# Kernel optimization log

Hardware: AMD Instinct MI355X
Metric: run time of the kernel (lower is better)

## Reference

```python
import jax, jax.numpy as jnp
import numpy as np

B, S, D_IN, D_OUT, H = 4, 2048, 1024, 1024, 16
HD = D_OUT // H  # 64


def setup_inputs() -> dict:
    key = jax.random.key(0)
    ks = jax.random.split(key, 6)
    s = 1.0 / np.sqrt(D_IN)
    return {
        "x": jax.random.normal(ks[0], (B, S, D_IN), dtype=jnp.float32),
        "Wq": jax.random.uniform(ks[1], (D_IN, D_OUT), jnp.float32, -s, s),
        "Wk": jax.random.uniform(ks[2], (D_IN, D_OUT), jnp.float32, -s, s),
        "Wv": jax.random.uniform(ks[3], (D_IN, D_OUT), jnp.float32, -s, s),
        "Wo": jax.random.uniform(ks[4], (D_OUT, D_OUT), jnp.float32, -s, s),
        "bo": jax.random.uniform(ks[5], (D_OUT,), jnp.float32, -s, s),
    }


def reference(x, Wq, Wk, Wv, Wo, bo):
    b, s, _ = x.shape
    # QKV projections -> [b, H, s, hd]
    def split_heads(t):
        return t.reshape(b, s, H, HD).transpose(0, 2, 1, 3)
    q = split_heads(x @ Wq)
    k = split_heads(x @ Wk)
    v = split_heads(x @ Wv)
    # attention scores [b, H, s, s]
    scores = jnp.einsum("bhqd,bhkd->bhqk", q, k)
    causal = jnp.triu(jnp.ones((s, s), dtype=bool), k=1)
    scores = jnp.where(causal, -jnp.inf, scores)
    attn = jax.nn.softmax(scores / np.sqrt(HD), axis=-1)
    ctx = jnp.einsum("bhqk,bhkd->bhqd", attn, v)
    ctx = ctx.transpose(0, 2, 1, 3).reshape(b, s, D_OUT)
    return ctx @ Wo + bo
```

## Files before the change

### kernel.cpp

```cpp
#include <hip/hip_runtime.h>

typedef __attribute__((ext_vector_type(8))) short bf16x8;
typedef __attribute__((ext_vector_type(4))) float f32x4;
typedef __attribute__((ext_vector_type(4))) unsigned uint4v;

#define SM_C 0.18033688011112042f
#define SM_M 20.0f
#define MFMA16 __builtin_amdgcn_mfma_f32_16x16x32_bf16

__device__ __forceinline__ unsigned short f2bf(float f) {
  unsigned u = __builtin_bit_cast(unsigned, f);
  u += 0x7fffu + ((u >> 16) & 1u);
  return (unsigned short)(u >> 16);
}

__device__ __forceinline__ unsigned cvtpk(float lo, float hi) {
  unsigned r;
  asm volatile("v_cvt_pk_bf16_f32 %0, %1, %2" : "=v"(r) : "v"(lo), "v"(hi));
  return r;
}

__device__ __forceinline__ void gload16(const void* g, void* lds) {
  __builtin_amdgcn_global_load_lds(
      (const __attribute__((address_space(1))) void*)g,
      (__attribute__((address_space(3))) void*)lds, 16, 0, 0);
}

#define BARRIER __builtin_amdgcn_s_barrier()
#define LGKM0 asm volatile("s_waitcnt lgkmcnt(0)" ::: "memory")
#define VM0 asm volatile("s_waitcnt vmcnt(0)" ::: "memory")

__global__ __launch_bounds__(256) void prep(const float* __restrict__ x,
                                            unsigned short* __restrict__ xb,
                                            const float* __restrict__ W0,
                                            const float* __restrict__ W1,
                                            const float* __restrict__ W2,
                                            const float* __restrict__ W3,
                                            unsigned short* __restrict__ WT) {
  __shared__ float tile[32][33];
  const int bid = blockIdx.x;
  if (bid < 2048) {
    int i = bid * 256 + threadIdx.x;
    for (; i < 2097152; i += 2048 * 256) {
      float4 v = ((const float4*)x)[i];
      unsigned long long packed = (unsigned long long)f2bf(v.x) |
                                  ((unsigned long long)f2bf(v.y) << 16) |
                                  ((unsigned long long)f2bf(v.z) << 32) |
                                  ((unsigned long long)f2bf(v.w) << 48);
      ((unsigned long long*)xb)[i] = packed;
    }
  } else {
    int b2 = bid - 2048;
    const int z = b2 >> 10;
    b2 &= 1023;
    const int bx = b2 & 31, by = b2 >> 5;
    const float* W = (z == 0) ? W0 : (z == 1) ? W1 : (z == 2) ? W2 : W3;
    unsigned short* WTo = WT + (size_t)z * 1048576;
    const int tx = threadIdx.x & 31, ty = threadIdx.x >> 5;
    const int xcol = bx * 32 + tx;
    for (int i = 0; i < 4; ++i) {
      int r = ty + i * 8;
      tile[r][tx] = W[(by * 32 + r) * 1024 + xcol];
    }
    __syncthreads();
    const int nx = by * 32 + tx;
    for (int i = 0; i < 4; ++i) {
      int r = ty + i * 8;
      WTo[(long)(bx * 32 + r) * 1024 + nx] = f2bf(tile[tx][r]);
    }
  }
}

template <int MODE>
__global__ __launch_bounds__(256) void gemm97(const unsigned short* __restrict__ A,
                                              const unsigned short* __restrict__ BT,
                                              unsigned short* __restrict__ Cb,
                                              float* __restrict__ Cf,
                                              const float* __restrict__ bias,
                                              int M, int N, int K) {
  __shared__ alignas(16) unsigned short As[2][128 * 64];
  __shared__ alignas(16) unsigned short Bs[2][128 * 64];

  const int nbn = N >> 7;
  const int tmg = (M >> 7) >> 3;
  const int cc = blockIdx.x >> 3, xc = blockIdx.x & 7;
  const int tm = xc * tmg + cc / nbn, tn = cc % nbn;

  const int t = threadIdx.x, l = t & 63, wid = t >> 6;
  const int wm = wid >> 1, wn = wid & 1;
  const int lr = l & 15, lg = l >> 4;

  f32x4 acc[4][4] = {};

  const int sq = t >> 3;
  const int sslot8 = ((t & 7) ^ (sq & 7)) * 8;
  const unsigned short* Ath = A + ((long)tm * 128 + sq) * K + sslot8;
  const unsigned short* Bth = BT + ((long)tn * 128 + sq) * K + sslot8;
  const int ldsoff = sq * 64 + (t & 7) * 8;

#define STG(buf, kt)                                                      \
  do {                                                                    \
    _Pragma("unroll") for (int q_ = 0; q_ < 4; ++q_) {                    \
      gload16(Ath + (long)(q_ * 32) * K + (kt) * 64,                      \
              &As[buf][q_ * 2048 + ldsoff]);                              \
      gload16(Bth + (long)(q_ * 32) * K + (kt) * 64,                      \
              &Bs[buf][q_ * 2048 + ldsoff]);                              \
    }                                                                     \
  } while (0)

  const int NT = K >> 6;
  STG(0, 0);
  VM0;
  BARRIER;

  const int offk0 = (lg ^ (lr & 7)) * 8;
  const int offk1 = ((4 + lg) ^ (lr & 7)) * 8;
  const int arow0 = (wm * 64 + lr) * 64;
  const int brow0 = (wn * 64 + lr) * 64;

  for (int tt = 0; tt < NT; ++tt) {
    const int cur = tt & 1;
    if (tt + 1 < NT) STG(cur ^ 1, tt + 1);

    const unsigned short* Ac = As[cur];
    const unsigned short* Bc = Bs[cur];
    bf16x8 af[4][2], bfr[4][2];
#pragma unroll
    for (int m = 0; m < 4; ++m) {
      const unsigned short* ap = Ac + arow0 + m * 1024;
      af[m][0] = *(const bf16x8*)(ap + offk0);
      af[m][1] = *(const bf16x8*)(ap + offk1);
    }
#pragma unroll
    for (int n = 0; n < 4; ++n) {
      const unsigned short* bp = Bc + brow0 + n * 1024;
      bfr[n][0] = *(const bf16x8*)(bp + offk0);
      bfr[n][1] = *(const bf16x8*)(bp + offk1);
    }
    LGKM0;
    __builtin_amdgcn_s_setprio(1);
#pragma unroll
    for (int m = 0; m < 4; ++m)
#pragma unroll
      for (int n = 0; n < 4; ++n) {
        acc[m][n] = MFMA16(af[m][0], bfr[n][0], acc[m][n], 0, 0, 0);
        acc[m][n] = MFMA16(af[m][1], bfr[n][1], acc[m][n], 0, 0, 0);
      }
    __builtin_amdgcn_s_setprio(0);

    if (tt + 1 < NT) {
      VM0;
      BARRIER;
    }
  }
#undef STG

  const long crow = (long)tm * 128 + wm * 64;
  const int ccolw = wn * 64;

  if constexpr (MODE == 1) {
#pragma unroll
    for (int m = 0; m < 4; ++m)
#pragma unroll
      for (int n = 0; n < 4; ++n)
#pragma unroll
        for (int r = 0; r < 4; ++r) {
          long row = crow + m * 16 + lg * 4 + r;
          int col = tn * 128 + ccolw + n * 16 + lr;
          Cf[row * N + col] = acc[m][n][r] + bias[col];
        }
  } else {
    if (tn < 16) {
      unsigned short* pl = Cb + ((tn < 8) ? 0 : 8388608);
      const int pc = (tn & 7) * 128 + ccolw + lr;
#pragma unroll
      for (int m = 0; m < 4; ++m)
#pragma unroll
        for (int n = 0; n < 4; ++n)
#pragma unroll
          for (int r = 0; r < 4; ++r) {
            long row = crow + m * 16 + lg * 4 + r;
            pl[row * 1024 + pc + n * 16] = f2bf(acc[m][n][r]);
          }
    } else {
      unsigned short* VtW = Cb + 16777216;
      const int bq = (tm >> 4) << 4;
      const int sbase = ((tm & 15) << 7) + wm * 64;
#pragma unroll
      for (int m = 0; m < 4; ++m) {
        const int srow_ = sbase + m * 16 + lg * 4;
        const int lwb = srow_ & 63;
        const int stt = srow_ >> 6;
        const int vp0 = (lwb & 32) | (((lwb >> 2) & 3) << 3) | (((lwb >> 4) & 1) << 2);
#pragma unroll
        for (int n = 0; n < 4; ++n) {
          const int vcol = (tn - 16) * 128 + ccolw + n * 16 + lr;
          const long vtrow = (long)(bq + (vcol >> 6)) * 64 + (vcol & 63);
          unsigned long long pk4 =
              (unsigned long long)f2bf(acc[m][n][0]) |
              ((unsigned long long)f2bf(acc[m][n][1]) << 16) |
              ((unsigned long long)f2bf(acc[m][n][2]) << 32) |
              ((unsigned long long)f2bf(acc[m][n][3]) << 48);
          *(unsigned long long*)(VtW + vtrow * 2048 + stt * 64 + vp0) = pk4;
        }
      }
    }
  }
}

template <int TWO>
__device__ __forceinline__ void attn_tile(
    const unsigned short* __restrict__ Kc, const unsigned short* __restrict__ Vc,
    int lr, int lg, bool mask0, bool mask1, int kv0, int q0row, int q1row,
    const bf16x8 (&qf)[2][2], f32x4 (&cacc)[2][4], float (&l_r)[2]) {
  constexpr int S0 = TWO ? 0 : 1;
  f32x4 p[2][4];
#pragma unroll
  for (int s = S0; s < 2; ++s)
#pragma unroll
    for (int g = 0; g < 4; ++g) p[s][g] = f32x4{0.f, 0.f, 0.f, 0.f};

  __builtin_amdgcn_s_setprio(1);
#pragma unroll
  for (int g = 0; g < 4; ++g) {
    const int key = g * 16 + lr;
    const int swz = (key & 7) << 3;
#pragma unroll
    for (int c = 0; c < 2; ++c) {
      bf16x8 kf = *(const bf16x8*)(Kc + key * 64 + ((c * 32 + lg * 8) ^ swz));
#pragma unroll
      for (int s = S0; s < 2; ++s)
        p[s][g] = MFMA16(kf, qf[s][c], p[s][g], 0, 0, 0);
    }
  }
  __builtin_amdgcn_s_setprio(0);

  if (TWO && mask0) {
#pragma unroll
    for (int g = 0; g < 4; ++g)
#pragma unroll
      for (int r = 0; r < 4; ++r)
        if (kv0 + g * 16 + lg * 4 + r > q0row) p[0][g][r] = -1e30f;
  }
  if (mask1) {
#pragma unroll
    for (int g = 0; g < 4; ++g)
#pragma unroll
      for (int r = 0; r < 4; ++r)
        if (kv0 + g * 16 + lg * 4 + r > q1row) p[1][g][r] = -1e30f;
  }

  const float SM_NMC = -SM_M * SM_C;
  unsigned pk[2][4][2];
#pragma unroll
  for (int s = S0; s < 2; ++s) {
    float e[4][4];
#pragma unroll
    for (int g = 0; g < 4; ++g)
#pragma unroll
      for (int r = 0; r < 4; ++r)
        e[g][r] = __builtin_amdgcn_exp2f(__builtin_fmaf(p[s][g][r], SM_C, SM_NMC));
    float t0 = (e[0][0] + e[0][1]) + (e[0][2] + e[0][3]);
    float t1 = (e[1][0] + e[1][1]) + (e[1][2] + e[1][3]);
    float t2 = (e[2][0] + e[2][1]) + (e[2][2] + e[2][3]);
    float t3 = (e[3][0] + e[3][1]) + (e[3][2] + e[3][3]);
    l_r[s] += (t0 + t1) + (t2 + t3);
#pragma unroll
    for (int g = 0; g < 4; ++g) {
      pk[s][g][0] = cvtpk(e[g][0], e[g][1]);
      pk[s][g][1] = cvtpk(e[g][2], e[g][3]);
    }
  }

#pragma unroll
  for (int sl = 0; sl < 2; ++sl) {
    bf16x8 vf[4];
#pragma unroll
    for (int n = 0; n < 4; ++n) {
      const int hd = n * 16 + lr;
      vf[n] = *(const bf16x8*)(Vc + hd * 64 + ((sl * 32 + lg * 8) ^ ((hd & 7) << 3)));
    }
    __builtin_amdgcn_s_setprio(1);
#pragma unroll
    for (int s = S0; s < 2; ++s) {
      uint4v pw = {pk[s][2 * sl][0], pk[s][2 * sl][1], pk[s][2 * sl + 1][0], pk[s][2 * sl + 1][1]};
      bf16x8 pa = __builtin_bit_cast(bf16x8, pw);
#pragma unroll
      for (int n = 0; n < 4; ++n)
        cacc[s][n] = MFMA16(pa, vf[n], cacc[s][n], 0, 0, 0);
    }
    __builtin_amdgcn_s_setprio(0);
  }
}

__global__ __launch_bounds__(256, 4) void flash_attn(const unsigned short* __restrict__ Qp,
                                                     const unsigned short* __restrict__ Kp,
                                                     const unsigned short* __restrict__ Vt,
                                                     unsigned short* __restrict__ Ctx) {
  __shared__ alignas(16) unsigned short Ks[2][64 * 64];
  __shared__ alignas(16) unsigned short Vs[2][64 * 64];
  const int bid = blockIdx.x;
  const int qt = bid >> 6;
  const int bh = bid & 63;
  const int b = bh >> 4, h = bh & 15;
  const int t = threadIdx.x, l = t & 63, w = t >> 6;
  const int lr = l & 15, lg = l >> 4;
  const long rowbase = (long)b * 2048;
  const int colbase = h * 64;
  const int q0 = qt * 64 + w * 16;
  const int q1 = (31 - qt) * 64 + w * 16;
  const int q0row = q0 + lr, q1row = q1 + lr;
  const int nkv = 32 - qt;

  bf16x8 qf[2][2];
#pragma unroll
  for (int c = 0; c < 2; ++c) {
    qf[0][c] = *(const bf16x8*)(Qp + (rowbase + q0 + lr) * 1024 + colbase + c * 32 + lg * 8);
    qf[1][c] = *(const bf16x8*)(Qp + (rowbase + q1 + lr) * 1024 + colbase + c * 32 + lg * 8);
  }

  f32x4 cacc[2][4];
  float l_r[2];
#pragma unroll
  for (int s = 0; s < 2; ++s) {
    l_r[s] = 0.f;
#pragma unroll
    for (int n = 0; n < 4; ++n) cacc[s][n] = f32x4{0.f, 0.f, 0.f, 0.f};
  }

  const int srow = w * 16 + (l >> 3);
  const int scol = (l & 7) * 8;
  const int kswz = scol ^ ((srow & 7) << 3);
  const unsigned short* kp = Kp + (rowbase + srow) * 1024 + colbase + kswz;
  const unsigned short* vp = Vt + ((long)(bh * 64 + srow)) * 2048 + kswz;
  unsigned short* ksd0 = &Ks[0][(w * 16) * 64];
  unsigned short* vsd0 = &Vs[0][(w * 16) * 64];

#define STAGE(buf)                                    \
  do {                                                \
    gload16(kp, ksd0 + (buf) * 4096);                 \
    gload16(kp + 8 * 1024, ksd0 + (buf) * 4096 + 512);\
    gload16(vp, vsd0 + (buf) * 4096);                 \
    gload16(vp + 8 * 2048, vsd0 + (buf) * 4096 + 512);\
    kp += 64 * 1024;                                  \
    vp += 64;                                         \
  } while (0)

#define TILE_WAIT(j)                                                          \
  do {                                                                        \
    if ((j) == nkv - 1) asm volatile("s_waitcnt vmcnt(0)" ::: "memory");      \
    else                asm volatile("s_waitcnt vmcnt(4)" ::: "memory");      \
    asm volatile("s_barrier" ::: "memory");                                   \
  } while (0)

  STAGE(0);
  STAGE(1);

  int j = 0;
  for (; j <= qt; ++j) {
    const int cur = j & 1;
    TILE_WAIT(j);
    attn_tile<1>(Ks[cur], Vs[cur], lr, lg, j == qt, false, j * 64, q0row, q1row,
                 qf, cacc, l_r);
    asm volatile("s_barrier" ::: "memory");
    if (j + 2 < nkv) STAGE(cur);
  }
  for (; j < nkv; ++j) {
    const int cur = j & 1;
    TILE_WAIT(j);
    attn_tile<0>(Ks[cur], Vs[cur], lr, lg, false, j == nkv - 1, j * 64, q0row, q1row,
                 qf, cacc, l_r);
    asm volatile("s_barrier" ::: "memory");
    if (j + 2 < nkv) STAGE(cur);
  }
#undef STAGE
#undef TILE_WAIT

#pragma unroll
  for (int s = 0; s < 2; ++s) {
    float rs = l_r[s];
    rs += __shfl_xor(rs, 16);
    rs += __shfl_xor(rs, 32);
    float invl = 1.f / rs;
    float ilq[4];
#pragma unroll
    for (int r = 0; r < 4; ++r) ilq[r] = __shfl(invl, lg * 20 + r);
    const int qs = (s == 0) ? q0 : q1;
#pragma unroll
    for (int n = 0; n < 4; ++n)
#pragma unroll
      for (int r = 0; r < 4; ++r) {
        long row = rowbase + qs + lg * 4 + r;
        Ctx[row * 1024 + colbase + n * 16 + lr] = f2bf(cacc[s][n][r] * ilq[r]);
      }
  }
}

extern "C" void kernel_launch(void* const* d_in, const int* in_sizes, int n_in,
                              void* d_out, int out_size, void* d_ws, size_t ws_size,
                              hipStream_t stream) {
  (void)in_sizes; (void)n_in; (void)out_size; (void)ws_size;
  const float* x  = (const float*)d_in[0];
  const float* Wq = (const float*)d_in[1];
  const float* Wk = (const float*)d_in[2];
  const float* Wv = (const float*)d_in[3];
  const float* Wo = (const float*)d_in[4];
  const float* bo = (const float*)d_in[5];
  float* out = (float*)d_out;

  unsigned short* ws = (unsigned short*)d_ws;
  unsigned short* xb  = ws;
  unsigned short* WqT = ws + 8388608;
  unsigned short* WoT = WqT + 3145728;
  unsigned short* QKV = WqT + 4194304;
  unsigned short* Qp  = QKV;
  unsigned short* Kp  = QKV + 8388608;
  unsigned short* Vt  = QKV + 16777216;
  unsigned short* Ctx = QKV + 25165824;

  prep<<<6144, 256, 0, stream>>>(x, xb, Wq, Wk, Wv, Wo, WqT);

  gemm97<0><<<1536, 256, 0, stream>>>(xb, WqT, QKV, nullptr, nullptr,
                                      8192, 3072, 1024);

  flash_attn<<<1024, 256, 0, stream>>>(Qp, Kp, Vt, Ctx);

  gemm97<1><<<512, 256, 0, stream>>>(Ctx, WoT, nullptr, out, bo,
                                     8192, 1024, 1024);
}
```

Measured before the change: 148.3 us.

## Shrink GEMM K-tile to 32 and merge flash-attention query tiles into 512-thread blocks

The GEMM kernel now stages K in 32-wide slices instead of 64, with a new XOR swizzle. This halves LDS use per block, allowing more resident blocks, at the cost of twice as many barrier-synchronised iterations. The flash attention kernel now launches 512-thread blocks, where two wave groups share each K/V tile across two query-tile pairs. This halves the number of blocks, and the block-to-head mapping is remapped per XCD to improve L2 locality. The risk is that waves with shorter causal ranges idle through barriers while the longer group finishes its tiles.

Measured after the change: 152.4 us. 2.7% more time.

```diff
diff --git a/kernel.cpp b/kernel.cpp
--- a/kernel.cpp
+++ b/kernel.cpp
@@ -72,14 +72,14 @@
 }
 
 template <int MODE>
-__global__ __launch_bounds__(256) void gemm97(const unsigned short* __restrict__ A,
+__global__ __launch_bounds__(256) void gemm32(const unsigned short* __restrict__ A,
                                               const unsigned short* __restrict__ BT,
                                               unsigned short* __restrict__ Cb,
                                               float* __restrict__ Cf,
                                               const float* __restrict__ bias,
                                               int M, int N, int K) {
-  __shared__ alignas(16) unsigned short As[2][128 * 64];
-  __shared__ alignas(16) unsigned short Bs[2][128 * 64];
+  __shared__ alignas(16) unsigned short As[2][128 * 32];
+  __shared__ alignas(16) unsigned short Bs[2][128 * 32];
 
   const int nbn = N >> 7;
   const int tmg = (M >> 7) >> 3;
@@ -92,31 +92,27 @@
 
   f32x4 acc[4][4] = {};
 
-  const int sq = t >> 3;
-  const int sslot8 = ((t & 7) ^ (sq & 7)) * 8;
-  const unsigned short* Ath = A + ((long)tm * 128 + sq) * K + sslot8;
-  const unsigned short* Bth = BT + ((long)tn * 128 + sq) * K + sslot8;
-  const int ldsoff = sq * 64 + (t & 7) * 8;
-
-#define STG(buf, kt)                                                      \
-  do {                                                                    \
-    _Pragma("unroll") for (int q_ = 0; q_ < 4; ++q_) {                    \
-      gload16(Ath + (long)(q_ * 32) * K + (kt) * 64,                      \
-              &As[buf][q_ * 2048 + ldsoff]);                              \
-      gload16(Bth + (long)(q_ * 32) * K + (kt) * 64,                      \
-              &Bs[buf][q_ * 2048 + ldsoff]);                              \
-    }                                                                     \
+  const int srow = t >> 2;
+  const int sslot8 = (((t & 3) ^ ((t >> 2) & 3) ^ ((t >> 4) & 3)) << 3);
+  const unsigned short* Ath = A + ((long)tm * 128 + srow) * K + sslot8;
+  const unsigned short* Bth = BT + ((long)tn * 128 + srow) * K + sslot8;
+
+#define STG(buf, kt)                                                \
+  do {                                                              \
+    gload16(Ath + (long)(kt) * 32, &As[buf][t * 8]);                \
+    gload16(Ath + (long)64 * K + (kt) * 32, &As[buf][2048 + t * 8]);\
+    gload16(Bth + (long)(kt) * 32, &Bs[buf][t * 8]);                \
+    gload16(Bth + (long)64 * K + (kt) * 32, &Bs[buf][2048 + t * 8]);\
   } while (0)
 
-  const int NT = K >> 6;
+  const int NT = K >> 5;
   STG(0, 0);
   VM0;
   BARRIER;
 
-  const int offk0 = (lg ^ (lr & 7)) * 8;
-  const int offk1 = ((4 + lg) ^ (lr & 7)) * 8;
-  const int arow0 = (wm * 64 + lr) * 64;
-  const int brow0 = (wn * 64 + lr) * 64;
+  const int offk = ((lg ^ (lr & 3) ^ ((lr >> 2) & 3)) << 3);
+  const int arow0 = (wm * 64 + lr) * 32;
+  const int brow0 = (wn * 64 + lr) * 32;
 
   for (int tt = 0; tt < NT; ++tt) {
     const int cur = tt & 1;
@@ -124,28 +120,20 @@
 
     const unsigned short* Ac = As[cur];
     const unsigned short* Bc = Bs[cur];
-    bf16x8 af[4][2], bfr[4][2];
-#pragma unroll
-    for (int m = 0; m < 4; ++m) {
-      const unsigned short* ap = Ac + arow0 + m * 1024;
-      af[m][0] = *(const bf16x8*)(ap + offk0);
-      af[m][1] = *(const bf16x8*)(ap + offk1);
-    }
-#pragma unroll
-    for (int n = 0; n < 4; ++n) {
-      const unsigned short* bp = Bc + brow0 + n * 1024;
-      bfr[n][0] = *(const bf16x8*)(bp + offk0);
-      bfr[n][1] = *(const bf16x8*)(bp + offk1);
-    }
+    bf16x8 af[4], bfr[4];
+#pragma unroll
+    for (int m = 0; m < 4; ++m)
+      af[m] = *(const bf16x8*)(Ac + arow0 + m * 512 + offk);
+#pragma unroll
+    for (int n = 0; n < 4; ++n)
+      bfr[n] = *(const bf16x8*)(Bc + brow0 + n * 512 + offk);
     LGKM0;
     __builtin_amdgcn_s_setprio(1);
 #pragma unroll
     for (int m = 0; m < 4; ++m)
 #pragma unroll
-      for (int n = 0; n < 4; ++n) {
-        acc[m][n] = MFMA16(af[m][0], bfr[n][0], acc[m][n], 0, 0, 0);
-        acc[m][n] = MFMA16(af[m][1], bfr[n][1], acc[m][n], 0, 0, 0);
-      }
+      for (int n = 0; n < 4; ++n)
+        acc[m][n] = MFMA16(af[m], bfr[n], acc[m][n], 0, 0, 0);
     __builtin_amdgcn_s_setprio(0);
 
     if (tt + 1 < NT) {
@@ -293,22 +281,27 @@
   }
 }
 
-__global__ __launch_bounds__(256, 4) void flash_attn(const unsigned short* __restrict__ Qp,
+__global__ __launch_bounds__(512, 4) void flash_attn(const unsigned short* __restrict__ Qp,
                                                      const unsigned short* __restrict__ Kp,
                                                      const unsigned short* __restrict__ Vt,
                                                      unsigned short* __restrict__ Ctx) {
   __shared__ alignas(16) unsigned short Ks[2][64 * 64];
   __shared__ alignas(16) unsigned short Vs[2][64 * 64];
   const int bid = blockIdx.x;
-  const int qt = bid >> 6;
-  const int bh = bid & 63;
+  const int xcd = bid & 7;
+  const int rest = bid >> 3;
+  const int bh = xcd * 8 + (rest & 7);
+  const int qt = rest >> 3;
   const int b = bh >> 4, h = bh & 15;
   const int t = threadIdx.x, l = t & 63, w = t >> 6;
+  const int wq = w & 3, grp = w >> 2;
   const int lr = l & 15, lg = l >> 4;
   const long rowbase = (long)b * 2048;
   const int colbase = h * 64;
-  const int q0 = qt * 64 + w * 16;
-  const int q1 = (31 - qt) * 64 + w * 16;
+  const int p0 = qt + (grp << 3);
+  const int p1 = 31 - qt - (grp << 3);
+  const int q0 = p0 * 64 + wq * 16;
+  const int q1 = p1 * 64 + wq * 16;
   const int q0row = q0 + lr, q1row = q1 + lr;
   const int nkv = 32 - qt;
 
@@ -328,48 +321,42 @@
     for (int n = 0; n < 4; ++n) cacc[s][n] = f32x4{0.f, 0.f, 0.f, 0.f};
   }
 
-  const int srow = w * 16 + (l >> 3);
-  const int scol = (l & 7) * 8;
+  const int srow = t >> 3;
+  const int scol = (t & 7) * 8;
   const int kswz = scol ^ ((srow & 7) << 3);
   const unsigned short* kp = Kp + (rowbase + srow) * 1024 + colbase + kswz;
   const unsigned short* vp = Vt + ((long)(bh * 64 + srow)) * 2048 + kswz;
-  unsigned short* ksd0 = &Ks[0][(w * 16) * 64];
-  unsigned short* vsd0 = &Vs[0][(w * 16) * 64];
-
-#define STAGE(buf)                                    \
-  do {                                                \
-    gload16(kp, ksd0 + (buf) * 4096);                 \
-    gload16(kp + 8 * 1024, ksd0 + (buf) * 4096 + 512);\
-    gload16(vp, vsd0 + (buf) * 4096);                 \
-    gload16(vp + 8 * 2048, vsd0 + (buf) * 4096 + 512);\
-    kp += 64 * 1024;                                  \
-    vp += 64;                                         \
+  unsigned short* ksd0 = &Ks[0][w * 512];
+  unsigned short* vsd0 = &Vs[0][w * 512];
+
+#define STAGE(buf)                     \
+  do {                                 \
+    gload16(kp, ksd0 + (buf) * 4096);  \
+    gload16(vp, vsd0 + (buf) * 4096);  \
+    kp += 64 * 1024;                   \
+    vp += 64;                          \
   } while (0)
 
 #define TILE_WAIT(j)                                                          \
   do {                                                                        \
     if ((j) == nkv - 1) asm volatile("s_waitcnt vmcnt(0)" ::: "memory");      \
-    else                asm volatile("s_waitcnt vmcnt(4)" ::: "memory");      \
+    else                asm volatile("s_waitcnt vmcnt(2)" ::: "memory");      \
     asm volatile("s_barrier" ::: "memory");                                   \
   } while (0)
 
   STAGE(0);
   STAGE(1);
 
-  int j = 0;
-  for (; j <= qt; ++j) {
+  for (int j = 0; j < nkv; ++j) {
     const int cur = j & 1;
     TILE_WAIT(j);
-    attn_tile<1>(Ks[cur], Vs[cur], lr, lg, j == qt, false, j * 64, q0row, q1row,
-                 qf, cacc, l_r);
-    asm volatile("s_barrier" ::: "memory");
-    if (j + 2 < nkv) STAGE(cur);
-  }
-  for (; j < nkv; ++j) {
-    const int cur = j & 1;
-    TILE_WAIT(j);
-    attn_tile<0>(Ks[cur], Vs[cur], lr, lg, false, j == nkv - 1, j * 64, q0row, q1row,
-                 qf, cacc, l_r);
+    if (j <= p0) {
+      attn_tile<1>(Ks[cur], Vs[cur], lr, lg, j == p0, j == p1, j * 64,
+                   q0row, q1row, qf, cacc, l_r);
+    } else if (j <= p1) {
+      attn_tile<0>(Ks[cur], Vs[cur], lr, lg, false, j == p1, j * 64,
+                   q0row, q1row, qf, cacc, l_r);
+    }
     asm volatile("s_barrier" ::: "memory");
     if (j + 2 < nkv) STAGE(cur);
   }
@@ -420,11 +407,11 @@
 
   prep<<<6144, 256, 0, stream>>>(x, xb, Wq, Wk, Wv, Wo, WqT);
 
-  gemm97<0><<<1536, 256, 0, stream>>>(xb, WqT, QKV, nullptr, nullptr,
+  gemm32<0><<<1536, 256, 0, stream>>>(xb, WqT, QKV, nullptr, nullptr,
                                       8192, 3072, 1024);
 
-  flash_attn<<<1024, 256, 0, stream>>>(Qp, Kp, Vt, Ctx);
-
-  gemm97<1><<<512, 256, 0, stream>>>(Ctx, WoT, nullptr, out, bo,
+  flash_attn<<<512, 512, 0, stream>>>(Qp, Kp, Vt, Ctx);
+
+  gemm32<1><<<512, 256, 0, stream>>>(Ctx, WoT, nullptr, out, bo,
                                      8192, 1024, 1024);
 }
```
